# Kernel tuning notes

Measured on AMD Instinct MI355X. Metric: run time of the kernel, lower is better.

## Reference

```python
import jax, jax.numpy as jnp
import numpy as np

N = 50000      # nodes
E = 800000     # edges (before self-loops)
IN = 256       # in_channels
OUT = 64       # out_channels per head
H = 4          # heads (layer 0)
LEAKY = 0.2    # PyG GATConv negative_slope default


def setup_inputs() -> dict:
    key = jax.random.key(0)
    ks = jax.random.split(key, 16)
    g = 0.1
    inp = {
        "x": jax.random.normal(ks[0], (N, IN), jnp.float32),
        "edge_index": jax.random.randint(ks[1], (2, E), 0, N, dtype=jnp.int32),
        # layer 0: in -> H*OUT, concat=True
        "W0": jax.random.normal(ks[2], (IN, H * OUT), jnp.float32) * g,
        "a_src0": jax.random.normal(ks[3], (H, OUT), jnp.float32) * g,
        "a_dst0": jax.random.normal(ks[4], (H, OUT), jnp.float32) * g,
        "b0": jnp.zeros((H * OUT,), jnp.float32),
        # layer 1: H*OUT -> OUT, heads=1, concat=False
        "W1": jax.random.normal(ks[5], (H * OUT, OUT), jnp.float32) * g,
        "a_src1": jax.random.normal(ks[6], (1, OUT), jnp.float32) * g,
        "a_dst1": jax.random.normal(ks[7], (1, OUT), jnp.float32) * g,
        "b1": jnp.zeros((OUT,), jnp.float32),
        # layer 2: H*OUT -> OUT (input is OUT from layer 1? no: layer1 outputs OUT)
        "W2": jax.random.normal(ks[8], (OUT, OUT), jnp.float32) * g,
        "a_src2": jax.random.normal(ks[9], (1, OUT), jnp.float32) * g,
        "a_dst2": jax.random.normal(ks[10], (1, OUT), jnp.float32) * g,
        "b2": jnp.zeros((OUT,), jnp.float32),
    }
    return inp


def _gat_layer(x, src, dst, W, a_s, a_d, b, heads, concat):
    """PyG GATConv: per-head linear, edge attention logits, segment softmax
    over incoming edges of each destination node, scatter-sum aggregate."""
    n = x.shape[0]
    h = (x @ W).reshape(n, heads, -1)                      # [N, H, C]
    al_s = (h * a_s).sum(-1)                               # [N, H]
    al_d = (h * a_d).sum(-1)                               # [N, H]
    e = jax.nn.leaky_relu(al_s[src] + al_d[dst], LEAKY)    # [E', H]
    m = jax.ops.segment_max(e, dst, num_segments=n)        # [N, H]
    ex = jnp.exp(e - m[dst])
    den = jax.ops.segment_sum(ex, dst, num_segments=n)     # [N, H]
    alpha = ex / (den[dst] + 1e-16)                        # [E', H]
    out = jax.ops.segment_sum(alpha[:, :, None] * h[src], dst, num_segments=n)  # [N,H,C]
    out = out.reshape(n, -1) if concat else out.mean(axis=1)
    return out + b


def reference(x, edge_index, W0, a_src0, a_dst0, b0, W1, a_src1, a_dst1, b1,
              W2, a_src2, a_dst2, b2):
    n = x.shape[0]
    loop = jnp.arange(n, dtype=edge_index.dtype)
    src = jnp.concatenate([edge_index[0], loop])   # PyG add_self_loops=True
    dst = jnp.concatenate([edge_index[1], loop])
    h = _gat_layer(x, src, dst, W0, a_src0, a_dst0, b0, H, True)
    h = jax.nn.elu(h)
    h = _gat_layer(h, src, dst, W1, a_src1, a_dst1, b1, 1, False)
    h = jax.nn.elu(h)
    h = _gat_layer(h, src, dst, W2, a_src2, a_dst2, b2, 1, False)
    h = jax.nn.elu(h)
    return h
```

## Files before the change

kernel.cpp:

```cpp
#include <hip/hip_runtime.h>
#include <hip/hip_bf16.h>


typedef unsigned short ushort_t;
typedef __attribute__((ext_vector_type(8))) short short8;
typedef __attribute__((ext_vector_type(4))) float f32x4;

__device__ __forceinline__ float elu_f(float x){ return x > 0.f ? x : expm1f(x); }
__device__ __forceinline__ float lrelu_f(float x){ return x > 0.f ? x : 0.2f * x; }
__device__ __forceinline__ ushort_t f2b(float f){
  union { float f; unsigned u; } v; v.f = f;
  unsigned r = v.u + 0x7fff + ((v.u >> 16) & 1);
  return (ushort_t)(r >> 16);
}
__device__ __forceinline__ float b2f_lo(unsigned v){
  union { unsigned u; float f; } c; c.u = v << 16; return c.f;
}
__device__ __forceinline__ float b2f_hi(unsigned v){
  union { unsigned u; float f; } c; c.u = v & 0xffff0000u; return c.f;
}

__global__ __launch_bounds__(256) void prep_kernel(const int* __restrict__ ei,
                                                   int* __restrict__ cnt,
                                                   const float4* __restrict__ x4,
                                                   ushort4* __restrict__ xb4, int n4,
                                                   const float* __restrict__ W0,
                                                   ushort_t* __restrict__ W0p,
                                                   const float* __restrict__ W1,
                                                   ushort_t* __restrict__ W1p,
                                                   const float* __restrict__ W2,
                                                   ushort_t* __restrict__ W2p,
                                                   int E, int Etot, int eb, int fb){
  int bid = blockIdx.x; int t = threadIdx.x;
  if(bid < eb){
    int e = bid * 256 + t;
    if(e < Etot){
      int d = (e < E) ? ei[E + e] : (e - E);
      atomicAdd(&cnt[d], 1);
    }
  } else if(bid < eb + fb){
    int i = (bid - eb) * 256 + t;
    if(i < n4){
      float4 v = x4[i];
      ushort4 o;
      o.x = f2b(v.x); o.y = f2b(v.y); o.z = f2b(v.z); o.w = f2b(v.w);
      xb4[i] = o;
    }
  } else {
    int r = bid - eb - fb;
    if(r < 256){
      int i = r * 256 + t; int k = i >> 8, n = i & 255;
      W0p[(size_t)n * 256 + k] = f2b(W0[i]);
    } else if(r < 320){
      int i = (r - 256) * 256 + t; int k = i >> 6, n = i & 63;
      W1p[(size_t)n * 256 + k] = f2b(W1[i]);
    } else {
      int i = (r - 320) * 256 + t; int k = i >> 6, n = i & 63;
      W2p[(size_t)n * 64 + k] = f2b(W2[i]);
    }
  }
}

__global__ __launch_bounds__(256) void blocksum_kernel(const int* __restrict__ cnt,
                                                       int* __restrict__ bsum, int N){
  __shared__ int sm[256];
  int t = threadIdx.x;
  int i = blockIdx.x * 256 + t;
  sm[t] = (i < N) ? cnt[i] : 0;
  __syncthreads();
  for(int off = 128; off > 0; off >>= 1){
    if(t < off) sm[t] += sm[t + off];
    __syncthreads();
  }
  if(t == 0) bsum[blockIdx.x] = sm[0];
}

__global__ __launch_bounds__(256) void scan2_kernel(const int* __restrict__ cnt,
                                                    const int* __restrict__ bsum,
                                                    int* __restrict__ rowptr,
                                                    int* __restrict__ cursor,
                                                    int N, int Etot, int nb){
  __shared__ int sm[256];
  __shared__ int spfx;
  int t = threadIdx.x;
  int c = blockIdx.x;
  sm[t] = (t < c && t < nb) ? bsum[t] : 0;
  __syncthreads();
  for(int off = 128; off > 0; off >>= 1){
    if(t < off) sm[t] += sm[t + off];
    __syncthreads();
  }
  if(t == 0) spfx = sm[0];
  __syncthreads();
  int pfx = spfx;
  __syncthreads();
  int i = c * 256 + t;
  int v = (i < N) ? cnt[i] : 0;
  sm[t] = v;
  __syncthreads();
  for(int off = 1; off < 256; off <<= 1){
    int x = 0;
    if(t >= off) x = sm[t - off];
    __syncthreads();
    sm[t] += x;
    __syncthreads();
  }
  if(i < N){
    int ex = sm[t] - v + pfx;
    rowptr[i] = ex;
    cursor[i] = ex;
    if(i == N - 1) rowptr[N] = Etot;
  }
}

__global__ __launch_bounds__(256) void scatter_kernel(const int* __restrict__ ei,
                                                      int* __restrict__ cursor,
                                                      int* __restrict__ esrc,
                                                      int E, int Etot){
  int e = blockIdx.x * 256 + threadIdx.x;
  if(e >= Etot) return;
  int s, d;
  if(e < E){ s = ei[e]; d = ei[E + e]; } else { s = e - E; d = s; }
  int pos = atomicAdd(&cursor[d], 1);
  esrc[pos] = s;
}

#define SKP 264
__global__ __launch_bounds__(256) void gemm0_kernel(const ushort_t* __restrict__ A,
                                                    const ushort_t* __restrict__ Bp,
                                                    ushort_t* __restrict__ h0b,
                                                    const float* __restrict__ asrc,
                                                    const float* __restrict__ adst,
                                                    float* __restrict__ als,
                                                    float* __restrict__ ald, int M){
  __shared__ ushort_t As[32 * SKP];
  int t = threadIdx.x;
  int row0 = blockIdx.x * 32;
  {
    int c = t;
    #pragma unroll
    for(int it = 0; it < 4; it++, c += 256){
      int r = c >> 5;
      int kc = (c & 31) << 3;
      int gr = row0 + r;
      short8 v = {};
      if(gr < M) v = *(const short8*)(A + (size_t)gr * 256 + kc);
      *(short8*)(As + r * SKP + kc) = v;
    }
  }
  __syncthreads();
  int wave = t >> 6, lane = t & 63;
  int m = lane & 15, q = lane >> 4;
  int colb = wave;
  const ushort_t* Bq = Bp + (size_t)(colb * 64 + m) * 256 + q * 8;
  const ushort_t* A0 = As + m * SKP + q * 8;
  const ushort_t* A1 = As + (16 + m) * SKP + q * 8;
  f32x4 acc[2][4] = {};
  for(int k0 = 0; k0 < 256; k0 += 32){
    short8 bv[4];
    #pragma unroll
    for(int j = 0; j < 4; j++) bv[j] = *(const short8*)(Bq + (size_t)j * 16 * 256 + k0);
    short8 a0 = *(const short8*)(A0 + k0);
    short8 a1 = *(const short8*)(A1 + k0);
    #pragma unroll
    for(int j = 0; j < 4; j++){
      acc[0][j] = __builtin_amdgcn_mfma_f32_16x16x32_bf16(a0, bv[j], acc[0][j], 0, 0, 0);
      acc[1][j] = __builtin_amdgcn_mfma_f32_16x16x32_bf16(a1, bv[j], acc[1][j], 0, 0, 0);
    }
  }
  #pragma unroll
  for(int rt = 0; rt < 2; rt++){
    #pragma unroll
    for(int j = 0; j < 4; j++){
      int col = colb * 64 + j * 16 + m;
      #pragma unroll
      for(int i = 0; i < 4; i++){
        int gr = row0 + rt * 16 + q * 4 + i;
        if(gr < M) h0b[(size_t)gr * 256 + col] = f2b(acc[rt][j][i]);
      }
    }
    float vs[4] = {0,0,0,0}, vd[4] = {0,0,0,0};
    #pragma unroll
    for(int j = 0; j < 4; j++){
      int col = colb * 64 + j * 16 + m;
      float a_s = asrc[col], a_d = adst[col];
      #pragma unroll
      for(int i = 0; i < 4; i++){
        vs[i] = fmaf(acc[rt][j][i], a_s, vs[i]);
        vd[i] = fmaf(acc[rt][j][i], a_d, vd[i]);
      }
    }
    #pragma unroll
    for(int off = 8; off > 0; off >>= 1){
      #pragma unroll
      for(int i = 0; i < 4; i++){
        vs[i] += __shfl_down(vs[i], off, 16);
        vd[i] += __shfl_down(vd[i], off, 16);
      }
    }
    if(m == 0){
      #pragma unroll
      for(int i = 0; i < 4; i++){
        int gr = row0 + rt * 16 + q * 4 + i;
        if(gr < M){
          als[(size_t)gr * 4 + colb] = vs[i];
          ald[(size_t)gr * 4 + colb] = vd[i];
        }
      }
    }
  }
}

__global__ __launch_bounds__(256, 8) void agg0_kernel(const int* __restrict__ rowptr,
                                                      const int* __restrict__ esrc,
                                                      const uint2* __restrict__ h0b2,
                                                      const float4* __restrict__ als4,
                                                      const float4* __restrict__ ald4,
                                                      const float4* __restrict__ b4,
                                                      uint2* __restrict__ out2, int N){
  int t = threadIdx.x;
  int lane = t & 63;
  int n = blockIdx.x * 4 + (t >> 6);
  if(n >= N) return;
  int h = lane >> 4;
  int beg = rowptr[n], end = rowptr[n + 1];
  float adh = ((const float*)(ald4 + n))[h];
  float4 acc = make_float4(0.f, 0.f, 0.f, 0.f);
  float den = 0.f;
  for(int c0 = beg; c0 < end; c0 += 16){
    int e = c0 + (lane & 15);
    int s = n; float w = 0.f;
    if(e < end){
      s = esrc[e];
      w = expf(lrelu_f(((const float*)(als4 + s))[h] + adh));
    }
    int rem = end - c0;
    if(rem > 16) rem = 16;
    #pragma unroll
    for(int g = 0; g < 4; g++){
      if(g * 4 < rem){
        #pragma unroll
        for(int ii = 0; ii < 4; ii++){
          int i = g * 4 + ii;
          int idx = (lane & 48) + i;
          int si = __shfl(s, idx, 64);
          float wi = __shfl(w, idx, 64);
          uint2 v = h0b2[((size_t)si << 6) + lane];
          acc.x = fmaf(wi, b2f_lo(v.x), acc.x);
          acc.y = fmaf(wi, b2f_hi(v.x), acc.y);
          acc.z = fmaf(wi, b2f_lo(v.y), acc.z);
          acc.w = fmaf(wi, b2f_hi(v.y), acc.w);
          den += wi;
        }
      }
    }
  }
  float inv = 1.f / (den + 1e-16f);
  float4 bb = b4[lane];
  float v0 = elu_f(acc.x * inv + bb.x);
  float v1 = elu_f(acc.y * inv + bb.y);
  float v2 = elu_f(acc.z * inv + bb.z);
  float v3 = elu_f(acc.w * inv + bb.w);
  uint2 o;
  o.x = (unsigned)f2b(v0) | ((unsigned)f2b(v1) << 16);
  o.y = (unsigned)f2b(v2) | ((unsigned)f2b(v3) << 16);
  out2[((size_t)n << 6) + lane] = o;
}

__global__ __launch_bounds__(256) void mfma_gemm(const ushort_t* __restrict__ A,
                                                 const ushort_t* __restrict__ Bp,
                                                 ushort_t* __restrict__ Cp,
                                                 const float* __restrict__ asrc,
                                                 const float* __restrict__ adst,
                                                 float* __restrict__ als,
                                                 float* __restrict__ ald,
                                                 int M, int K, int NC){
  int wave = threadIdx.x >> 6;
  int lane = threadIdx.x & 63;
  int tile0 = (blockIdx.x * 4 + wave) * 2;
  if(tile0 * 16 >= M) return;
  bool two = (tile0 + 1) * 16 < M;
  int m = lane & 15, q = lane >> 4;
  const ushort_t* Ab = A + (size_t)(tile0 * 16 + m) * K + q * 8;
  const ushort_t* Bq = Bp + (size_t)m * K + q * 8;
  f32x4 acc[2][4] = {};
  for(int k0 = 0; k0 < K; k0 += 32){
    short8 bv[4];
    #pragma unroll
    for(int j = 0; j < 4; j++) bv[j] = *(const short8*)(Bq + (size_t)j * 16 * K + k0);
    short8 a0 = *(const short8*)(Ab + k0);
    #pragma unroll
    for(int j = 0; j < 4; j++)
      acc[0][j] = __builtin_amdgcn_mfma_f32_16x16x32_bf16(a0, bv[j], acc[0][j], 0, 0, 0);
    if(two){
      short8 a1 = *(const short8*)(Ab + (size_t)16 * K + k0);
      #pragma unroll
      for(int j = 0; j < 4; j++)
        acc[1][j] = __builtin_amdgcn_mfma_f32_16x16x32_bf16(a1, bv[j], acc[1][j], 0, 0, 0);
    }
  }
  #pragma unroll
  for(int r = 0; r < 2; r++){
    if(r == 1 && !two) break;
    int rowt = tile0 + r;
    #pragma unroll
    for(int j = 0; j < 4; j++){
      int col = j * 16 + m;
      #pragma unroll
      for(int i = 0; i < 4; i++){
        int rr = rowt * 16 + q * 4 + i;
        Cp[(size_t)rr * NC + col] = f2b(acc[r][j][i]);
      }
    }
    float vs[4] = {0,0,0,0}, vd[4] = {0,0,0,0};
    #pragma unroll
    for(int j = 0; j < 4; j++){
      int col = j * 16 + m;
      float a_s = asrc[col], a_d = adst[col];
      #pragma unroll
      for(int i = 0; i < 4; i++){
        vs[i] = fmaf(acc[r][j][i], a_s, vs[i]);
        vd[i] = fmaf(acc[r][j][i], a_d, vd[i]);
      }
    }
    #pragma unroll
    for(int off = 8; off > 0; off >>= 1){
      #pragma unroll
      for(int i = 0; i < 4; i++){
        vs[i] += __shfl_down(vs[i], off, 16);
        vd[i] += __shfl_down(vd[i], off, 16);
      }
    }
    if(m == 0){
      #pragma unroll
      for(int i = 0; i < 4; i++){
        int rr = rowt * 16 + q * 4 + i;
        als[rr] = vs[i];
        ald[rr] = vd[i];
      }
    }
  }
}

#define H2S 72
__global__ __launch_bounds__(256, 8) void agg1g2_kernel(const int* __restrict__ rowptr,
                                                        const int* __restrict__ esrc,
                                                        const unsigned* __restrict__ g1b,
                                                        const float* __restrict__ als1,
                                                        const float* __restrict__ ald1,
                                                        const float* __restrict__ b1,
                                                        const ushort_t* __restrict__ W2p,
                                                        const float* __restrict__ as2,
                                                        const float* __restrict__ ad2,
                                                        ushort_t* __restrict__ g2b,
                                                        float* __restrict__ als2,
                                                        float* __restrict__ ald2, int N){
  __shared__ ushort_t Hs[16 * H2S];
  __shared__ float aps[4][16], apd[4][16];
  int t = threadIdx.x;
  int wave = t >> 6, lane = t & 63;
  int nbase = blockIdx.x * 16;
  int half = lane >> 5;
  int p = lane & 31;
  for(int j = 0; j < 4; j++){
    int n = nbase + wave * 4 + j;
    int nl = wave * 4 + j;
    if(n < N){
      int beg = rowptr[n], end = rowptr[n + 1];
      float ad = ald1[n];
      float a0 = 0.f, a1 = 0.f, den = 0.f;
      for(int c0 = beg; c0 < end; c0 += 32){
        int e = c0 + p;
        int s = n; float w = 0.f;
        if(e < end){
          s = esrc[e];
          w = expf(lrelu_f(als1[s] + ad));
        }
        int rem = end - c0;
        if(rem > 32) rem = 32;
        int npair = (rem + 1) >> 1;
        #pragma unroll
        for(int g = 0; g < 4; g++){
          if(g * 4 < npair){
            #pragma unroll
            for(int ii = 0; ii < 4; ii++){
              int i = g * 4 + ii;
              int idx = 2 * i + half;
              int si = __shfl(s, idx, 64);
              float wi = __shfl(w, idx, 64);
              unsigned v = g1b[((size_t)si << 5) + p];
              a0 = fmaf(wi, b2f_lo(v), a0);
              a1 = fmaf(wi, b2f_hi(v), a1);
              den += wi;
            }
          }
        }
      }
      a0 += __shfl_xor(a0, 32, 64);
      a1 += __shfl_xor(a1, 32, 64);
      den += __shfl_xor(den, 32, 64);
      float inv = 1.f / (den + 1e-16f);
      float2 bb = ((const float2*)b1)[p];
      if(half == 0){
        unsigned o = (unsigned)f2b(elu_f(a0 * inv + bb.x)) |
                     ((unsigned)f2b(elu_f(a1 * inv + bb.y)) << 16);
        *(unsigned*)(Hs + nl * H2S + p * 2) = o;
      }
    }
  }
  __syncthreads();
  int m = lane & 15, q = lane >> 4;
  const ushort_t* Bw = W2p + (size_t)(wave * 16 + m) * 64 + q * 8;
  const ushort_t* Aw = Hs + m * H2S + q * 8;
  f32x4 acc = {};
  #pragma unroll
  for(int k0 = 0; k0 < 64; k0 += 32){
    short8 av = *(const short8*)(Aw + k0);
    short8 bv = *(const short8*)(Bw + k0);
    acc = __builtin_amdgcn_mfma_f32_16x16x32_bf16(av, bv, acc, 0, 0, 0);
  }
  float a_s = as2[wave * 16 + m], a_d = ad2[wave * 16 + m];
  float vs[4], vd[4];
  #pragma unroll
  for(int i = 0; i < 4; i++){
    int gn = nbase + q * 4 + i;
    if(gn < N) g2b[(size_t)gn * 64 + wave * 16 + m] = f2b(acc[i]);
    vs[i] = acc[i] * a_s;
    vd[i] = acc[i] * a_d;
  }
  #pragma unroll
  for(int off = 8; off > 0; off >>= 1){
    #pragma unroll
    for(int i = 0; i < 4; i++){
      vs[i] += __shfl_down(vs[i], off, 16);
      vd[i] += __shfl_down(vd[i], off, 16);
    }
  }
  if(m == 0){
    #pragma unroll
    for(int i = 0; i < 4; i++){
      aps[wave][q * 4 + i] = vs[i];
      apd[wave][q * 4 + i] = vd[i];
    }
  }
  __syncthreads();
  if(t < 16){
    int gn = nbase + t;
    if(gn < N){
      als2[gn] = aps[0][t] + aps[1][t] + aps[2][t] + aps[3][t];
      ald2[gn] = apd[0][t] + apd[1][t] + apd[2][t] + apd[3][t];
    }
  }
}

__global__ __launch_bounds__(256, 8) void aggF_kernel(const int* __restrict__ rowptr,
                                                      const int* __restrict__ esrc,
                                                      const unsigned* __restrict__ gb,
                                                      const float* __restrict__ als,
                                                      const float* __restrict__ ald,
                                                      const float* __restrict__ b,
                                                      float2* __restrict__ outp, int N){
  int t = threadIdx.x;
  int lane = t & 63;
  int n = blockIdx.x * 4 + (t >> 6);
  if(n >= N) return;
  int half = lane >> 5;
  int p = lane & 31;
  int beg = rowptr[n], end = rowptr[n + 1];
  float ad = ald[n];
  float a0 = 0.f, a1 = 0.f, den = 0.f;
  for(int c0 = beg; c0 < end; c0 += 32){
    int e = c0 + p;
    int s = n; float w = 0.f;
    if(e < end){
      s = esrc[e];
      w = expf(lrelu_f(als[s] + ad));
    }
    int rem = end - c0;
    if(rem > 32) rem = 32;
    int npair = (rem + 1) >> 1;
    #pragma unroll
    for(int g = 0; g < 4; g++){
      if(g * 4 < npair){
        #pragma unroll
        for(int ii = 0; ii < 4; ii++){
          int i = g * 4 + ii;
          int idx = 2 * i + half;
          int si = __shfl(s, idx, 64);
          float wi = __shfl(w, idx, 64);
          unsigned v = gb[((size_t)si << 5) + p];
          a0 = fmaf(wi, b2f_lo(v), a0);
          a1 = fmaf(wi, b2f_hi(v), a1);
          den += wi;
        }
      }
    }
  }
  a0 += __shfl_xor(a0, 32, 64);
  a1 += __shfl_xor(a1, 32, 64);
  den += __shfl_xor(den, 32, 64);
  float inv = 1.f / (den + 1e-16f);
  float2 bb = ((const float2*)b)[p];
  if(half == 0){
    float2 o;
    o.x = elu_f(a0 * inv + bb.x);
    o.y = elu_f(a1 * inv + bb.y);
    outp[((size_t)n << 5) + p] = o;
  }
}

extern "C" void kernel_launch(void* const* d_in, const int* in_sizes, int n_in,
                              void* d_out, int out_size, void* d_ws, size_t ws_size,
                              hipStream_t stream){
  const float* x   = (const float*)d_in[0];
  const int*   ei  = (const int*)d_in[1];
  const float* W0  = (const float*)d_in[2];
  const float* as0 = (const float*)d_in[3];
  const float* ad0 = (const float*)d_in[4];
  const float* b0  = (const float*)d_in[5];
  const float* W1  = (const float*)d_in[6];
  const float* as1 = (const float*)d_in[7];
  const float* ad1 = (const float*)d_in[8];
  const float* b1  = (const float*)d_in[9];
  const float* W2  = (const float*)d_in[10];
  const float* as2 = (const float*)d_in[11];
  const float* ad2 = (const float*)d_in[12];
  const float* b2  = (const float*)d_in[13];
  int N = in_sizes[0] / 256;
  int E = in_sizes[1] / 2;
  int Etot = E + N;

  size_t off = 0;
  auto alc = [&](size_t bytes) -> char* {
    char* p = (char*)d_ws + off;
    off += (bytes + 255) & ~(size_t)255;
    return p;
  };
  ushort_t* xb    = (ushort_t*)alc((size_t)N * 256 * 2);
  ushort_t* h0b   = (ushort_t*)alc((size_t)N * 256 * 2);
  float*    als   = (float*)alc((size_t)N * 4 * 4);
  float*    ald   = (float*)alc((size_t)N * 4 * 4);
  float*    als1  = (float*)alc((size_t)N * 4);
  float*    ald1  = (float*)alc((size_t)N * 4);
  float*    als2  = (float*)alc((size_t)N * 4);
  float*    ald2  = (float*)alc((size_t)N * 4);
  int*      esrc  = (int*)alc((size_t)Etot * 4);
  int*      rowptr= (int*)alc((size_t)(N + 1) * 4);
  int*      cnt   = (int*)alc((size_t)N * 4);
  int*      cursor= (int*)alc((size_t)N * 4);
  int*      bsum  = (int*)alc(256 * 4);
  ushort_t* W0p   = (ushort_t*)alc(256 * 256 * 2);
  ushort_t* W1p   = (ushort_t*)alc(256 * 64 * 2);
  ushort_t* W2p   = (ushort_t*)alc(64 * 64 * 2);

  ushort_t* h1b = xb;
  ushort_t* g1b = h0b;
  ushort_t* g2b = xb;

  int nb = (N + 255) / 256;
  int eb = (Etot + 255) / 256;
  int fb = (N * 64 + 255) / 256;
  int g0b = (N + 31) / 32;
  int rb = ((N / 16) + 7) / 8;
  int tb = (N + 15) / 16;
  int ab = (N + 3) / 4;

  hipMemsetAsync(cnt, 0, (size_t)N * 4, stream);
  prep_kernel<<<eb + fb + 336, 256, 0, stream>>>(ei, cnt, (const float4*)x,
                                                 (ushort4*)xb, N * 64,
                                                 W0, W0p, W1, W1p, W2, W2p,
                                                 E, Etot, eb, fb);
  blocksum_kernel<<<nb, 256, 0, stream>>>(cnt, bsum, N);
  scan2_kernel<<<nb, 256, 0, stream>>>(cnt, bsum, rowptr, cursor, N, Etot, nb);
  scatter_kernel<<<eb, 256, 0, stream>>>(ei, cursor, esrc, E, Etot);

  gemm0_kernel<<<g0b, 256, 0, stream>>>(xb, W0p, h0b, as0, ad0, als, ald, N);
  agg0_kernel<<<ab, 256, 0, stream>>>(rowptr, esrc, (const uint2*)h0b,
                                      (const float4*)als, (const float4*)ald,
                                      (const float4*)b0, (uint2*)h1b, N);

  mfma_gemm<<<rb, 256, 0, stream>>>(h1b, W1p, g1b, as1, ad1, als1, ald1,
                                    N, 256, 64);

  agg1g2_kernel<<<tb, 256, 0, stream>>>(rowptr, esrc, (const unsigned*)g1b,
                                        als1, ald1, b1, W2p, as2, ad2,
                                        g2b, als2, ald2, N);

  aggF_kernel<<<ab, 256, 0, stream>>>(rowptr, esrc, (const unsigned*)g2b,
                                      als2, ald2, b2, (float2*)d_out, N);
}
```

Baseline: 376.3 us.

## Process four nodes per wave in 64-wide aggregation kernels with batched gathers

```diff
diff --git a/kernel.cpp b/kernel.cpp
--- a/kernel.cpp
+++ b/kernel.cpp
@@ -239,18 +239,23 @@
     #pragma unroll
     for(int g = 0; g < 4; g++){
       if(g * 4 < rem){
+        int si[4]; float wi[4]; uint2 v[4];
         #pragma unroll
         for(int ii = 0; ii < 4; ii++){
-          int i = g * 4 + ii;
-          int idx = (lane & 48) + i;
-          int si = __shfl(s, idx, 64);
-          float wi = __shfl(w, idx, 64);
-          uint2 v = h0b2[((size_t)si << 6) + lane];
-          acc.x = fmaf(wi, b2f_lo(v.x), acc.x);
-          acc.y = fmaf(wi, b2f_hi(v.x), acc.y);
-          acc.z = fmaf(wi, b2f_lo(v.y), acc.z);
-          acc.w = fmaf(wi, b2f_hi(v.y), acc.w);
-          den += wi;
+          int idx = (lane & 48) + g * 4 + ii;
+          si[ii] = __shfl(s, idx, 64);
+          wi[ii] = __shfl(w, idx, 64);
+        }
+        #pragma unroll
+        for(int ii = 0; ii < 4; ii++)
+          v[ii] = h0b2[((size_t)si[ii] << 6) + lane];
+        #pragma unroll
+        for(int ii = 0; ii < 4; ii++){
+          acc.x = fmaf(wi[ii], b2f_lo(v[ii].x), acc.x);
+          acc.y = fmaf(wi[ii], b2f_hi(v[ii].x), acc.y);
+          acc.z = fmaf(wi[ii], b2f_lo(v[ii].y), acc.z);
+          acc.w = fmaf(wi[ii], b2f_hi(v[ii].y), acc.w);
+          den += wi[ii];
         }
       }
     }
@@ -345,7 +350,7 @@
 #define H2S 72
 __global__ __launch_bounds__(256, 8) void agg1g2_kernel(const int* __restrict__ rowptr,
                                                         const int* __restrict__ esrc,
-                                                        const unsigned* __restrict__ g1b,
+                                                        const uint2* __restrict__ g1b2,
                                                         const float* __restrict__ als1,
                                                         const float* __restrict__ ald1,
                                                         const float* __restrict__ b1,
@@ -360,53 +365,51 @@
   int t = threadIdx.x;
   int wave = t >> 6, lane = t & 63;
   int nbase = blockIdx.x * 16;
-  int half = lane >> 5;
-  int p = lane & 31;
-  for(int j = 0; j < 4; j++){
-    int n = nbase + wave * 4 + j;
-    int nl = wave * 4 + j;
-    if(n < N){
-      int beg = rowptr[n], end = rowptr[n + 1];
-      float ad = ald1[n];
-      float a0 = 0.f, a1 = 0.f, den = 0.f;
-      for(int c0 = beg; c0 < end; c0 += 32){
-        int e = c0 + p;
-        int s = n; float w = 0.f;
-        if(e < end){
-          s = esrc[e];
-          w = expf(lrelu_f(als1[s] + ad));
-        }
-        int rem = end - c0;
-        if(rem > 32) rem = 32;
-        int npair = (rem + 1) >> 1;
-        #pragma unroll
-        for(int g = 0; g < 4; g++){
-          if(g * 4 < npair){
-            #pragma unroll
-            for(int ii = 0; ii < 4; ii++){
-              int i = g * 4 + ii;
-              int idx = 2 * i + half;
-              int si = __shfl(s, idx, 64);
-              float wi = __shfl(w, idx, 64);
-              unsigned v = g1b[((size_t)si << 5) + p];
-              a0 = fmaf(wi, b2f_lo(v), a0);
-              a1 = fmaf(wi, b2f_hi(v), a1);
-              den += wi;
-            }
+  int g = lane >> 4;
+  int p = lane & 15;
+  int n = nbase + wave * 4 + g;
+  int nl = wave * 4 + g;
+  if(n < N){
+    int beg = rowptr[n], end = rowptr[n + 1];
+    float ad = ald1[n];
+    float4 acc = make_float4(0.f, 0.f, 0.f, 0.f);
+    float den = 0.f;
+    for(int c0 = beg; c0 < end; c0 += 16){
+      int e = c0 + p;
+      int s = n; float w = 0.f;
+      if(e < end){
+        s = esrc[e];
+        w = expf(lrelu_f(als1[s] + ad));
+      }
+      int rem = end - c0;
+      if(rem > 16) rem = 16;
+      #pragma unroll
+      for(int gg = 0; gg < 4; gg++){
+        if(gg * 4 < rem){
+          #pragma unroll
+          for(int ii = 0; ii < 4; ii++){
+            int i = gg * 4 + ii;
+            int idx = (lane & 48) + i;
+            int si = __shfl(s, idx, 64);
+            float wi = __shfl(w, idx, 64);
+            uint2 v = g1b2[((size_t)si << 4) + p];
+            acc.x = fmaf(wi, b2f_lo(v.x), acc.x);
+            acc.y = fmaf(wi, b2f_hi(v.x), acc.y);
+            acc.z = fmaf(wi, b2f_lo(v.y), acc.z);
+            acc.w = fmaf(wi, b2f_hi(v.y), acc.w);
+            den += wi;
           }
         }
       }
-      a0 += __shfl_xor(a0, 32, 64);
-      a1 += __shfl_xor(a1, 32, 64);
-      den += __shfl_xor(den, 32, 64);
-      float inv = 1.f / (den + 1e-16f);
-      float2 bb = ((const float2*)b1)[p];
-      if(half == 0){
-        unsigned o = (unsigned)f2b(elu_f(a0 * inv + bb.x)) |
-                     ((unsigned)f2b(elu_f(a1 * inv + bb.y)) << 16);
-        *(unsigned*)(Hs + nl * H2S + p * 2) = o;
-      }
-    }
+    }
+    float inv = 1.f / (den + 1e-16f);
+    float4 bb = ((const float4*)b1)[p];
+    unsigned o0 = (unsigned)f2b(elu_f(acc.x * inv + bb.x)) |
+                  ((unsigned)f2b(elu_f(acc.y * inv + bb.y)) << 16);
+    unsigned o1 = (unsigned)f2b(elu_f(acc.z * inv + bb.z)) |
+                  ((unsigned)f2b(elu_f(acc.w * inv + bb.w)) << 16);
+    uint2 ov; ov.x = o0; ov.y = o1;
+    *(uint2*)(Hs + nl * H2S + p * 4) = ov;
   }
   __syncthreads();
   int m = lane & 15, q = lane >> 4;
@@ -455,21 +458,22 @@
 
 __global__ __launch_bounds__(256, 8) void aggF_kernel(const int* __restrict__ rowptr,
                                                       const int* __restrict__ esrc,
-                                                      const unsigned* __restrict__ gb,
+                                                      const uint2* __restrict__ gb2,
                                                       const float* __restrict__ als,
                                                       const float* __restrict__ ald,
                                                       const float* __restrict__ b,
-                                                      float2* __restrict__ outp, int N){
+                                                      float4* __restrict__ outp, int N){
   int t = threadIdx.x;
   int lane = t & 63;
-  int n = blockIdx.x * 4 + (t >> 6);
+  int g = lane >> 4;
+  int p = lane & 15;
+  int n = blockIdx.x * 16 + (t >> 6) * 4 + g;
   if(n >= N) return;
-  int half = lane >> 5;
-  int p = lane & 31;
   int beg = rowptr[n], end = rowptr[n + 1];
   float ad = ald[n];
-  float a0 = 0.f, a1 = 0.f, den = 0.f;
-  for(int c0 = beg; c0 < end; c0 += 32){
+  float4 acc = make_float4(0.f, 0.f, 0.f, 0.f);
+  float den = 0.f;
+  for(int c0 = beg; c0 < end; c0 += 16){
     int e = c0 + p;
     int s = n; float w = 0.f;
     if(e < end){
@@ -477,36 +481,34 @@
       w = expf(lrelu_f(als[s] + ad));
     }
     int rem = end - c0;
-    if(rem > 32) rem = 32;
-    int npair = (rem + 1) >> 1;
-    #pragma unroll
-    for(int g = 0; g < 4; g++){
-      if(g * 4 < npair){
+    if(rem > 16) rem = 16;
+    #pragma unroll
+    for(int gg = 0; gg < 4; gg++){
+      if(gg * 4 < rem){
         #pragma unroll
         for(int ii = 0; ii < 4; ii++){
-          int i = g * 4 + ii;
-          int idx = 2 * i + half;
+          int i = gg * 4 + ii;
+          int idx = (lane & 48) + i;
           int si = __shfl(s, idx, 64);
           float wi = __shfl(w, idx, 64);
-          unsigned v = gb[((size_t)si << 5) + p];
-          a0 = fmaf(wi, b2f_lo(v), a0);
-          a1 = fmaf(wi, b2f_hi(v), a1);
+          uint2 v = gb2[((size_t)si << 4) + p];
+          acc.x = fmaf(wi, b2f_lo(v.x), acc.x);
+          acc.y = fmaf(wi, b2f_hi(v.x), acc.y);
+          acc.z = fmaf(wi, b2f_lo(v.y), acc.z);
+          acc.w = fmaf(wi, b2f_hi(v.y), acc.w);
           den += wi;
         }
       }
     }
   }
-  a0 += __shfl_xor(a0, 32, 64);
-  a1 += __shfl_xor(a1, 32, 64);
-  den += __shfl_xor(den, 32, 64);
   float inv = 1.f / (den + 1e-16f);
-  float2 bb = ((const float2*)b)[p];
-  if(half == 0){
-    float2 o;
-    o.x = elu_f(a0 * inv + bb.x);
-    o.y = elu_f(a1 * inv + bb.y);
-    outp[((size_t)n << 5) + p] = o;
-  }
+  float4 bb = ((const float4*)b)[p];
+  float4 o;
+  o.x = elu_f(acc.x * inv + bb.x);
+  o.y = elu_f(acc.y * inv + bb.y);
+  o.z = elu_f(acc.z * inv + bb.z);
+  o.w = elu_f(acc.w * inv + bb.w);
+  outp[((size_t)n << 4) + p] = o;
 }
 
 extern "C" void kernel_launch(void* const* d_in, const int* in_sizes, int n_in,
@@ -564,6 +566,7 @@
   int rb = ((N / 16) + 7) / 8;
   int tb = (N + 15) / 16;
   int ab = (N + 3) / 4;
+  int ab16 = (N + 15) / 16;
 
   hipMemsetAsync(cnt, 0, (size_t)N * 4, stream);
   prep_kernel<<<eb + fb + 336, 256, 0, stream>>>(ei, cnt, (const float4*)x,
@@ -582,10 +585,10 @@
   mfma_gemm<<<rb, 256, 0, stream>>>(h1b, W1p, g1b, as1, ad1, als1, ald1,
                                     N, 256, 64);
 
-  agg1g2_kernel<<<tb, 256, 0, stream>>>(rowptr, esrc, (const unsigned*)g1b,
+  agg1g2_kernel<<<tb, 256, 0, stream>>>(rowptr, esrc, (const uint2*)g1b,
                                         als1, ald1, b1, W2p, as2, ad2,
                                         g2b, als2, ald2, N);
 
-  aggF_kernel<<<ab, 256, 0, stream>>>(rowptr, esrc, (const unsigned*)g2b,
-                                      als2, ald2, b2, (float2*)d_out, N);
-}
+  aggF_kernel<<<ab16, 256, 0, stream>>>(rowptr, esrc, (const uint2*)g2b,
+                                        als2, ald2, b2, (float4*)d_out, N);
+}
```

New measurement: 366.3 us. 2.7% less time.
